# Kernel tuning notes

Hardware: AMD Instinct MI355X
Metric: run time of the kernel (lower is better)

## Reference

```python
import jax, jax.numpy as jnp
import numpy as np
import math

B, S, D, H = 2, 2048, 1024, 16
HD = D // H  # 64 head features


def setup_inputs() -> dict:
    key = jax.random.key(0)
    ks = jax.random.split(key, 6)
    x = jax.random.normal(ks[0], (B, S, D), jnp.float32)
    wq = jax.random.normal(ks[1], (D, D), jnp.float32) * 0.02
    wk = jax.random.normal(ks[2], (D, D), jnp.float32) * 0.02
    wv = jax.random.normal(ks[3], (D, D), jnp.float32) * 0.02
    wo = jax.random.normal(ks[4], (D, D), jnp.float32) * 0.02
    # Llama-style RoPE frequencies: unit-modulus complex per (pos, pair),
    # stored as separate cos/sin arrays of shape [S, HD//2].
    inv_freq = 1.0 / (10000.0 ** (jnp.arange(0, HD, 2, dtype=jnp.float32) / HD))
    ang = jnp.arange(S, dtype=jnp.float32)[:, None] * inv_freq[None, :]
    freq_cos = jnp.cos(ang)
    freq_sin = jnp.sin(ang)
    # realistic padding: each sequence keeps a random prefix of at least S//2 tokens
    lengths = jax.random.randint(ks[5], (B,), S // 2, S + 1)
    padding_mask = (jnp.arange(S)[None, :] < lengths[:, None]).astype(jnp.int32)
    return dict(x=x, wq=wq, wk=wk, wv=wv, wo=wo,
                freq_cos=freq_cos, freq_sin=freq_sin, padding_mask=padding_mask)


def _apply_rope(t, cos, sin):
    # t: [B, S, H, HD]; cos/sin: [S, HD//2]
    tr = t.reshape(t.shape[:-1] + (HD // 2, 2))
    t0, t1 = tr[..., 0], tr[..., 1]
    c = cos[None, :, None, :]
    s = sin[None, :, None, :]
    o0 = t0 * c - t1 * s  # real part of complex multiply
    o1 = t0 * s + t1 * c  # imag part
    return jnp.stack([o0, o1], axis=-1).reshape(t.shape)


def reference(x, wq, wk, wv, wo, freq_cos, freq_sin, padding_mask):
    # QKV projections (torch Linear: y = x @ W.T, no bias)
    q = (x @ wq.T).reshape(B, S, H, HD)
    k = (x @ wk.T).reshape(B, S, H, HD)
    v = (x @ wv.T).reshape(B, S, H, HD)
    q = _apply_rope(q, freq_cos, freq_sin)
    k = _apply_rope(k, freq_cos, freq_sin)
    q = jnp.transpose(q, (0, 2, 1, 3))  # [B,H,S,HD]
    k = jnp.transpose(k, (0, 2, 1, 3))
    v = jnp.transpose(v, (0, 2, 1, 3))
    # NOTE: original scales by sqrt(n_features), not sqrt(head_dim)
    scores = jnp.einsum('bhqd,bhkd->bhqk', q, k) / math.sqrt(D)
    bias = jnp.where(padding_mask[:, None, None, :] == 0,
                     jnp.float32(-jnp.inf), jnp.float32(0.0))
    p = jax.nn.softmax(scores + bias, axis=-1)
    out = jnp.einsum('bhqk,bhkd->bhqd', p, v)
    out = jnp.transpose(out, (0, 2, 1, 3)).reshape(B, S, D)
    return out @ wo.T
```

## Files before the change

kernel.cpp:

```cpp
#include <hip/hip_runtime.h>
#include <hip/hip_bf16.h>
#include <stdint.h>

typedef unsigned short u16;
typedef __attribute__((ext_vector_type(8))) short bf16x8;
typedef __attribute__((ext_vector_type(4))) float f32x4;
typedef __attribute__((ext_vector_type(16))) float f32x16;

__device__ __forceinline__ u16 f2bf(float f) {
  union { float f; uint32_t u; } a; a.f = f;
  return (u16)((a.u + 0x7FFFu + ((a.u >> 16) & 1u)) >> 16);
}

__device__ __forceinline__ void gload_lds16(const void* g, void* l) {
  auto* gp = (__attribute__((address_space(1))) void*)(uintptr_t)g;
  auto* lp = (__attribute__((address_space(3))) void*)(uintptr_t)l;
  __builtin_amdgcn_global_load_lds(gp, lp, 16, 0, 0);
}

__device__ __forceinline__ float exp2_fast(float x) {
  float r;
  asm("v_exp_f32 %0, %1" : "=v"(r) : "v"(x));
  return r;
}

#define CVTPK(d, a, b) asm("v_cvt_pk_bf16_f32 %0, %1, %2" : "=v"(d) : "v"(a), "v"(b))
#define SWAP32(a, b)   asm("v_permlane32_swap_b32 %0, %1" : "+v"(a), "+v"(b))

__global__ void cvt_kernel(const float4* __restrict__ x, const float4* __restrict__ wq,
                           const float4* __restrict__ wk, const float4* __restrict__ wv,
                           const float4* __restrict__ wo,
                           ushort4* __restrict__ xb, ushort4* __restrict__ wqkv,
                           ushort4* __restrict__ wob) {
  const int XN = (2 * 2048 * 1024) / 4;
  const int WN = (1024 * 1024) / 4;
  const int total = XN + 4 * WN;
  for (int i = blockIdx.x * 256 + threadIdx.x; i < total; i += gridDim.x * 256) {
    float4 v; ushort4* dst;
    if (i < XN) { v = x[i]; dst = xb + i; }
    else {
      int j = i - XN; int m = j >> 18; int o = j & (WN - 1);
      const float4* src = (m == 0) ? wq : (m == 1) ? wk : (m == 2) ? wv : wo;
      v = src[o];
      dst = (m < 3) ? (wqkv + j) : (wob + o);
    }
    ushort4 r; r.x = f2bf(v.x); r.y = f2bf(v.y); r.z = f2bf(v.z); r.w = f2bf(v.w);
    *dst = r;
  }
}

__global__ void len_kernel(const int* __restrict__ mask, int* __restrict__ lens) {
  __shared__ int red[256];
  int b = blockIdx.x, s = 0;
  for (int i = threadIdx.x; i < 2048; i += 256) s += mask[b * 2048 + i];
  red[threadIdx.x] = s;
  __syncthreads();
  if (threadIdx.x < 64) {
    int v = red[threadIdx.x] + red[threadIdx.x + 64] + red[threadIdx.x + 128] + red[threadIdx.x + 192];
    #pragma unroll
    for (int o = 32; o > 0; o >>= 1) v += __shfl_down(v, o);
    if (threadIdx.x == 0) lens[b] = v;
  }
}

template <int MODE>
__global__ __launch_bounds__(256, 2)
void gemm_bt(const u16* __restrict__ A, const u16* __restrict__ Bm,
             int M, int N, float* __restrict__ outf,
             u16* __restrict__ Qb, u16* __restrict__ Kb, u16* __restrict__ VbT,
             const float* __restrict__ cosT, const float* __restrict__ sinT) {
  const int K = 1024;
  __shared__ alignas(16) u16 Alds[128 * 32];
  __shared__ alignas(16) u16 Blds[128 * 32];
  const int tid = threadIdx.x, lane = tid & 63, wid = tid >> 6;
  const int nTm = M >> 7;
  const int m0 = (blockIdx.x % nTm) << 7;
  const int n0 = (blockIdx.x / nTm) << 7;
  const int wm = (wid >> 1) << 6, wn = (wid & 1) << 6;
  const int lr = lane & 15, lg = lane >> 4;

  f32x4 acc[4][4];
  #pragma unroll
  for (int i = 0; i < 4; ++i)
    #pragma unroll
    for (int j = 0; j < 4; ++j)
      #pragma unroll
      for (int e = 0; e < 4; ++e) acc[i][j][e] = 0.0f;

  const int r4 = tid >> 2, c4 = (tid & 3) * 8;
  const u16* ag0 = A + (int64_t)(m0 + r4) * K + c4;
  const u16* ag1 = A + (int64_t)(m0 + 64 + r4) * K + c4;
  const u16* bg0 = Bm + (int64_t)(n0 + r4) * K + c4;
  const u16* bg1 = Bm + (int64_t)(n0 + 64 + r4) * K + c4;
  u16* al0 = &Alds[(tid & 192) * 8];
  u16* al1 = &Alds[(256 + (tid & 192)) * 8];
  u16* bl0 = &Blds[(tid & 192) * 8];
  u16* bl1 = &Blds[(256 + (tid & 192)) * 8];

  for (int kt = 0; kt < K / 32; ++kt) {
    const int ko = kt * 32;
    gload_lds16(ag0 + ko, al0);
    gload_lds16(ag1 + ko, al1);
    gload_lds16(bg0 + ko, bl0);
    gload_lds16(bg1 + ko, bl1);
    __syncthreads();
    bf16x8 af[4], bfm[4];
    #pragma unroll
    for (int i = 0; i < 4; ++i) af[i] = *(const bf16x8*)&Alds[(wm + i * 16 + lr) * 32 + lg * 8];
    #pragma unroll
    for (int i = 0; i < 4; ++i) bfm[i] = *(const bf16x8*)&Blds[(wn + i * 16 + lr) * 32 + lg * 8];
    #pragma unroll
    for (int mi = 0; mi < 4; ++mi)
      #pragma unroll
      for (int ni = 0; ni < 4; ++ni)
        acc[mi][ni] = __builtin_amdgcn_mfma_f32_16x16x32_bf16(af[mi], bfm[ni], acc[mi][ni], 0, 0, 0);
    __syncthreads();
  }

  if (MODE == 0) {
    #pragma unroll
    for (int mi = 0; mi < 4; ++mi)
      #pragma unroll
      for (int r = 0; r < 4; ++r) {
        const int row = m0 + wm + mi * 16 + lg * 4 + r;
        float* orow = outf + (int64_t)row * N + n0 + wn + lr;
        #pragma unroll
        for (int ni = 0; ni < 4; ++ni) orow[ni * 16] = acc[mi][ni][r];
      }
  } else {
    #pragma unroll
    for (int mi = 0; mi < 4; ++mi) {
      #pragma unroll
      for (int r = 0; r < 4; ++r) {
        const int row = m0 + wm + mi * 16 + lg * 4 + r;
        const int bb = row >> 11, ss = row & 2047;
        #pragma unroll
        for (int ni = 0; ni < 4; ++ni) {
          const int n = n0 + wn + ni * 16 + lr;
          float v = acc[mi][ni][r];
          if (n < 2048) {
            float partner = __shfl_xor(v, 1);
            const int ii = (n >> 1) & 31;
            const float c = cosT[ss * 32 + ii];
            const float sn = sinT[ss * 32 + ii];
            float rv = (n & 1) ? (partner * sn + v * c) : (v * c - partner * sn);
            const int h = (n >> 6) & 15, d = n & 63;
            const int idx = ((bb * 16 + h) * 2048 + ss) * 64 + d;
            if (n < 1024) Qb[idx] = f2bf(rv * 0.0450842298f);
            else          Kb[idx] = f2bf(rv);
          } else {
            const int n2 = n - 2048;
            const int h = n2 >> 6, d = n2 & 63;
            VbT[((int64_t)(bb * 16 + h) * 64 + d) * 2048 + ss] = f2bf(v);
          }
        }
      }
    }
  }
}

__global__ __launch_bounds__(256, 2)
void attn_kernel(const u16* __restrict__ Qb, const u16* __restrict__ Kb,
                 const u16* __restrict__ VbT, u16* __restrict__ attnb,
                 const int* __restrict__ lens) {
  __shared__ alignas(16) u16 Klds[2][64 * 64];
  __shared__ alignas(16) u16 Vlds[2][64 * 64];
  const int tid = threadIdx.x, lane = tid & 63, wid = tid >> 6;
  const int hi = lane >> 5, ql = lane & 31;
  const int bh = blockIdx.x >> 4;
  const int len = lens[bh >> 4];
  const int qrow = (blockIdx.x & 15) * 128 + wid * 32 + ql;

  bf16x8 qf[4];
  const u16* qptr = Qb + ((int64_t)bh * 2048 + qrow) * 64 + hi * 8;
  #pragma unroll
  for (int c = 0; c < 4; ++c) qf[c] = *(const bf16x8*)(qptr + c * 16);

  const int srow = tid >> 3, schunk = (tid & 7) ^ (srow & 7);
  const u16* kg = Kb + ((int64_t)bh * 2048 + srow) * 64 + schunk * 8;
  const u16* vg = VbT + ((int64_t)bh * 64 + srow) * 2048 + schunk * 8;
  const int dstoff = wid * 512;

  f32x16 oacc[2];
  #pragma unroll
  for (int r = 0; r < 16; ++r) { oacc[0][r] = 0.0f; oacc[1][r] = 0.0f; }
  float mrun = -1e30f, lrun = 0.0f;

  const int nt = (len + 63) >> 6;
  gload_lds16(kg,             &Klds[0][dstoff]);
  gload_lds16(kg + 32 * 64,   &Klds[0][2048 + dstoff]);
  gload_lds16(vg,             &Vlds[0][dstoff]);
  gload_lds16(vg + 32 * 2048, &Vlds[0][2048 + dstoff]);
  __syncthreads();

  const u16* kgn = kg + 64 * 64;
  const u16* vgn = vg + 64;

  for (int t = 0; t < nt; ++t) {
    const int bu = t & 1;
    if (t + 1 < nt) {
      gload_lds16(kgn,             &Klds[bu ^ 1][dstoff]);
      gload_lds16(kgn + 32 * 64,   &Klds[bu ^ 1][2048 + dstoff]);
      gload_lds16(vgn,             &Vlds[bu ^ 1][dstoff]);
      gload_lds16(vgn + 32 * 2048, &Vlds[bu ^ 1][2048 + dstoff]);
    }
    kgn += 64 * 64; vgn += 64;

    f32x16 s0, s1;
    #pragma unroll
    for (int r = 0; r < 16; ++r) { s0[r] = 0.0f; s1[r] = 0.0f; }
    __builtin_amdgcn_s_setprio(1);
    #pragma unroll
    for (int c = 0; c < 4; ++c) {
      const int slot = (((2 * c + hi) ^ (ql & 7)) * 8);
      bf16x8 kf0 = *(const bf16x8*)&Klds[bu][ql * 64 + slot];
      bf16x8 kf1 = *(const bf16x8*)&Klds[bu][(32 + ql) * 64 + slot];
      s0 = __builtin_amdgcn_mfma_f32_32x32x16_bf16(kf0, qf[c], s0, 0, 0, 0);
      s1 = __builtin_amdgcn_mfma_f32_32x32x16_bf16(kf1, qf[c], s1, 0, 0, 0);
    }
    __builtin_amdgcn_s_setprio(0);

    const int k0 = t * 64;
    if (k0 + 64 > len) {
      #pragma unroll
      for (int r = 0; r < 16; ++r) {
        const int key = k0 + (r & 3) + 8 * (r >> 2) + 4 * hi;
        if (key >= len) s0[r] = -1e30f;
        if (key + 32 >= len) s1[r] = -1e30f;
      }
    }

    float ma = fmaxf(s0[0], s1[0]), mb = fmaxf(s0[1], s1[1]);
    float mc = fmaxf(s0[2], s1[2]), md = fmaxf(s0[3], s1[3]);
    #pragma unroll
    for (int r = 4; r < 16; r += 4) {
      ma = fmaxf(ma, fmaxf(s0[r], s1[r]));
      mb = fmaxf(mb, fmaxf(s0[r + 1], s1[r + 1]));
      mc = fmaxf(mc, fmaxf(s0[r + 2], s1[r + 2]));
      md = fmaxf(md, fmaxf(s0[r + 3], s1[r + 3]));
    }
    float mx = fmaxf(fmaxf(ma, mb), fmaxf(mc, md));
    mx = fmaxf(mx, __shfl_xor(mx, 32));
    if (!__all(mx - mrun <= 11.0f)) {
      const float mnew = fmaxf(mrun, mx);
      const float sc = exp2_fast(mrun - mnew);
      #pragma unroll
      for (int r = 0; r < 16; ++r) { oacc[0][r] *= sc; oacc[1][r] *= sc; }
      lrun *= sc;
      mrun = mnew;
    }
    float p[32];
    float ps0 = 0.0f, ps1 = 0.0f, ps2 = 0.0f, ps3 = 0.0f;
    #pragma unroll
    for (int r = 0; r < 16; r += 4) {
      p[r]      = exp2_fast(s0[r] - mrun);
      p[r + 1]  = exp2_fast(s0[r + 1] - mrun);
      p[r + 2]  = exp2_fast(s0[r + 2] - mrun);
      p[r + 3]  = exp2_fast(s0[r + 3] - mrun);
      p[16 + r]     = exp2_fast(s1[r] - mrun);
      p[16 + r + 1] = exp2_fast(s1[r + 1] - mrun);
      p[16 + r + 2] = exp2_fast(s1[r + 2] - mrun);
      p[16 + r + 3] = exp2_fast(s1[r + 3] - mrun);
      ps0 += p[r] + p[16 + r];
      ps1 += p[r + 1] + p[16 + r + 1];
      ps2 += p[r + 2] + p[16 + r + 2];
      ps3 += p[r + 3] + p[16 + r + 3];
    }
    float psum = (ps0 + ps1) + (ps2 + ps3);
    psum += __shfl_xor(psum, 32);
    lrun += psum;

    bf16x8 pfrag[4];
    #pragma unroll
    for (int ks = 0; ks < 4; ++ks) {
      uint32_t a0, a1, a2, a3;
      CVTPK(a0, p[8 * ks + 0], p[8 * ks + 1]);
      CVTPK(a1, p[8 * ks + 2], p[8 * ks + 3]);
      CVTPK(a2, p[8 * ks + 4], p[8 * ks + 5]);
      CVTPK(a3, p[8 * ks + 6], p[8 * ks + 7]);
      SWAP32(a0, a2);
      SWAP32(a1, a3);
      union { uint32_t u[4]; bf16x8 v; } pw;
      pw.u[0] = a0; pw.u[1] = a1; pw.u[2] = a2; pw.u[3] = a3;
      pfrag[ks] = pw.v;
    }

    __builtin_amdgcn_s_setprio(1);
    #pragma unroll
    for (int dc = 0; dc < 2; ++dc) {
      const int drow = dc * 32 + ql;
      #pragma unroll
      for (int ks = 0; ks < 4; ++ks) {
        const int slot = (((2 * ks + hi) ^ (ql & 7)) * 8);
        bf16x8 vf = *(const bf16x8*)&Vlds[bu][drow * 64 + slot];
        oacc[dc] = __builtin_amdgcn_mfma_f32_32x32x16_bf16(vf, pfrag[ks], oacc[dc], 0, 0, 0);
      }
    }
    __builtin_amdgcn_s_setprio(0);
    __syncthreads();
  }

  const float inv = 1.0f / lrun;
  u16* outp = attnb + ((int64_t)((bh >> 4) * 2048 + qrow)) * 1024 + (bh & 15) * 64;
  #pragma unroll
  for (int dc = 0; dc < 2; ++dc)
    #pragma unroll
    for (int g = 0; g < 4; ++g) {
      ushort4 w;
      w.x = f2bf(oacc[dc][4 * g + 0] * inv);
      w.y = f2bf(oacc[dc][4 * g + 1] * inv);
      w.z = f2bf(oacc[dc][4 * g + 2] * inv);
      w.w = f2bf(oacc[dc][4 * g + 3] * inv);
      *(ushort4*)(outp + dc * 32 + 8 * g + 4 * hi) = w;
    }
}

extern "C" void kernel_launch(void* const* d_in, const int* in_sizes, int n_in,
                              void* d_out, int out_size, void* d_ws, size_t ws_size,
                              hipStream_t stream) {
  const float* x    = (const float*)d_in[0];
  const float* wq   = (const float*)d_in[1];
  const float* wk   = (const float*)d_in[2];
  const float* wv   = (const float*)d_in[3];
  const float* wo   = (const float*)d_in[4];
  const float* fcos = (const float*)d_in[5];
  const float* fsin = (const float*)d_in[6];
  const int*   pmsk = (const int*)d_in[7];
  float* out = (float*)d_out;

  char* ws = (char*)d_ws;
  u16* XB    = (u16*)(ws);
  u16* WQKV  = (u16*)(ws + (size_t)8  * 1048576);
  u16* WOB   = (u16*)(ws + (size_t)14 * 1048576);
  u16* QB    = (u16*)(ws + (size_t)16 * 1048576);
  u16* KB    = (u16*)(ws + (size_t)24 * 1048576);
  u16* VBT   = (u16*)(ws + (size_t)32 * 1048576);
  u16* ATTNB = (u16*)(ws + (size_t)40 * 1048576);
  int* LENS  = (int*)(ws + (size_t)48 * 1048576);

  cvt_kernel<<<2048, 256, 0, stream>>>((const float4*)x, (const float4*)wq,
                                       (const float4*)wk, (const float4*)wv,
                                       (const float4*)wo, (ushort4*)XB,
                                       (ushort4*)WQKV, (ushort4*)WOB);
  len_kernel<<<2, 256, 0, stream>>>(pmsk, LENS);
  gemm_bt<1><<<768, 256, 0, stream>>>(XB, WQKV, 4096, 3072, nullptr,
                                      QB, KB, VBT, fcos, fsin);
  attn_kernel<<<512, 256, 0, stream>>>(QB, KB, VBT, ATTNB, LENS);
  gemm_bt<0><<<256, 256, 0, stream>>>(ATTNB, WOB, 4096, 1024, out,
                                      nullptr, nullptr, nullptr, nullptr, nullptr);
}
```

Measured before the change: 122.5 us.

## Replace GEMMs with 8-wave double-buffered swizzled-LDS kernel and split-K output projection

Replaces the simple 128x128 GEMM with an 8-wave, 512-thread kernel. It uses 256-wide N tiles and K=64 steps, XOR-swizzled LDS staging, double buffering with interleaved global-to-LDS loads and MFMA quads, setprio, and XCD-aware block remapping. The QKV projection uses 256x256 tiles. The output projection uses 128x256 tiles with split-K over two slices, accumulated with float atomics after a memset. The aim is to raise MFMA utilisation and hide load latency. In exchange it adds an extra memset, atomic traffic, and non-deterministic summation order.

```diff
diff --git a/kernel.cpp b/kernel.cpp
--- a/kernel.cpp
+++ b/kernel.cpp
@@ -26,6 +26,8 @@
 
 #define CVTPK(d, a, b) asm("v_cvt_pk_bf16_f32 %0, %1, %2" : "=v"(d) : "v"(a), "v"(b))
 #define SWAP32(a, b)   asm("v_permlane32_swap_b32 %0, %1" : "+v"(a), "+v"(b))
+#define BARRIER() do { asm volatile("" ::: "memory"); __builtin_amdgcn_s_barrier(); asm volatile("" ::: "memory"); } while (0)
+#define WAITVM(n) asm volatile("s_waitcnt vmcnt(" #n ")" ::: "memory")
 
 __global__ void cvt_kernel(const float4* __restrict__ x, const float4* __restrict__ wq,
                            const float4* __restrict__ wk, const float4* __restrict__ wv,
@@ -63,80 +65,144 @@
   }
 }
 
-template <int MODE>
-__global__ __launch_bounds__(256, 2)
-void gemm_bt(const u16* __restrict__ A, const u16* __restrict__ Bm,
-             int M, int N, float* __restrict__ outf,
-             u16* __restrict__ Qb, u16* __restrict__ Kb, u16* __restrict__ VbT,
-             const float* __restrict__ cosT, const float* __restrict__ sinT) {
-  const int K = 1024;
-  __shared__ alignas(16) u16 Alds[128 * 32];
-  __shared__ alignas(16) u16 Blds[128 * 32];
+template <int BM, int MODE>
+__global__ __launch_bounds__(512, 2)
+void gemm8(const u16* __restrict__ A, const u16* __restrict__ Bm,
+           int nTm, int nit,
+           float* __restrict__ outf,
+           u16* __restrict__ Qb, u16* __restrict__ Kb, u16* __restrict__ VbT,
+           const float* __restrict__ cosT, const float* __restrict__ sinT) {
+  constexpr int MREP = BM / 32;
+  constexpr int MH   = MREP / 2;
+  constexpr int HA   = BM / 2;
+  constexpr int LA   = BM / 128;
+  extern __shared__ __align__(16) u16 lds[];
+  u16* SA = lds;
+  u16* SB = lds + 2 * BM * 64;
+
   const int tid = threadIdx.x, lane = tid & 63, wid = tid >> 6;
-  const int nTm = M >> 7;
-  const int m0 = (blockIdx.x % nTm) << 7;
-  const int n0 = (blockIdx.x / nTm) << 7;
-  const int wm = (wid >> 1) << 6, wn = (wid & 1) << 6;
+  const int wm = wid >> 2, wn = wid & 3;
   const int lr = lane & 15, lg = lane >> 4;
 
-  f32x4 acc[4][4];
+  const int cpx = gridDim.x >> 3;
+  const int bid = (blockIdx.x & 7) * cpx + (blockIdx.x >> 3);
+  const int m0 = (bid % nTm) * BM;
+  const int n0 = (bid / nTm) * 256;
+  const int kt0 = blockIdx.y * nit * 2;
+
+  const int srow = tid >> 3;
+  const int sslot = (tid & 7) ^ (srow & 7);
+  const u16* gA = A + (int64_t)(m0 + srow) * 1024 + sslot * 8 + kt0 * 64;
+  const u16* gB = Bm + (int64_t)(n0 + srow) * 1024 + sslot * 8 + kt0 * 64;
+  const int sdst = wid * 512;
+
+#define STAGE_A(h, kt) do { \
+    _Pragma("unroll") for (int j = 0; j < LA; ++j) \
+      gload_lds16(gA + (int64_t)((h) * HA + j * 64) * 1024 + (kt) * 64, \
+                  &SA[(((kt) & 1) * BM + (h) * HA) * 64 + sdst + j * 4096]); } while (0)
+#define STAGE_B(h, kt) do { \
+    _Pragma("unroll") for (int j = 0; j < 2; ++j) \
+      gload_lds16(gB + (int64_t)((h) * 128 + j * 64) * 1024 + (kt) * 64, \
+                  &SB[(((kt) & 1) * 256 + (h) * 128) * 64 + sdst + j * 4096]); } while (0)
+#define RD_A(par, mh, dst) do { \
+    _Pragma("unroll") for (int mi = 0; mi < MH; ++mi) \
+    _Pragma("unroll") for (int ks = 0; ks < 2; ++ks) { \
+      const int row = wm * HA + (mh) * (BM / 4) + mi * 16 + lr; \
+      dst[mi][ks] = *(const bf16x8*)&SA[((par) * BM + row) * 64 + (((ks * 4 + lg) ^ (row & 7)) * 8)]; } } while (0)
+#define RD_B(par, nh, dst) do { \
+    _Pragma("unroll") for (int nj = 0; nj < 2; ++nj) \
+    _Pragma("unroll") for (int ks = 0; ks < 2; ++ks) { \
+      const int row = wn * 64 + (nh) * 32 + nj * 16 + lr; \
+      dst[nj][ks] = *(const bf16x8*)&SB[((par) * 256 + row) * 64 + (((ks * 4 + lg) ^ (row & 7)) * 8)]; } } while (0)
+#define QUAD(mh, nh, af, bf) do { \
+    __builtin_amdgcn_s_setprio(1); \
+    _Pragma("unroll") for (int ks = 0; ks < 2; ++ks) \
+    _Pragma("unroll") for (int mi = 0; mi < MH; ++mi) \
+    _Pragma("unroll") for (int nj = 0; nj < 2; ++nj) \
+      acc[(mh) * MH + mi][(nh) * 2 + nj] = __builtin_amdgcn_mfma_f32_16x16x32_bf16( \
+          af[mi][ks], bf[nj][ks], acc[(mh) * MH + mi][(nh) * 2 + nj], 0, 0, 0); \
+    __builtin_amdgcn_s_setprio(0); } while (0)
+
+  f32x4 acc[MREP][4];
   #pragma unroll
-  for (int i = 0; i < 4; ++i)
+  for (int i = 0; i < MREP; ++i)
     #pragma unroll
     for (int j = 0; j < 4; ++j)
       #pragma unroll
       for (int e = 0; e < 4; ++e) acc[i][j][e] = 0.0f;
 
-  const int r4 = tid >> 2, c4 = (tid & 3) * 8;
-  const u16* ag0 = A + (int64_t)(m0 + r4) * K + c4;
-  const u16* ag1 = A + (int64_t)(m0 + 64 + r4) * K + c4;
-  const u16* bg0 = Bm + (int64_t)(n0 + r4) * K + c4;
-  const u16* bg1 = Bm + (int64_t)(n0 + 64 + r4) * K + c4;
-  u16* al0 = &Alds[(tid & 192) * 8];
-  u16* al1 = &Alds[(256 + (tid & 192)) * 8];
-  u16* bl0 = &Blds[(tid & 192) * 8];
-  u16* bl1 = &Blds[(256 + (tid & 192)) * 8];
-
-  for (int kt = 0; kt < K / 32; ++kt) {
-    const int ko = kt * 32;
-    gload_lds16(ag0 + ko, al0);
-    gload_lds16(ag1 + ko, al1);
-    gload_lds16(bg0 + ko, bl0);
-    gload_lds16(bg1 + ko, bl1);
-    __syncthreads();
-    bf16x8 af[4], bfm[4];
-    #pragma unroll
-    for (int i = 0; i < 4; ++i) af[i] = *(const bf16x8*)&Alds[(wm + i * 16 + lr) * 32 + lg * 8];
-    #pragma unroll
-    for (int i = 0; i < 4; ++i) bfm[i] = *(const bf16x8*)&Blds[(wn + i * 16 + lr) * 32 + lg * 8];
-    #pragma unroll
-    for (int mi = 0; mi < 4; ++mi)
-      #pragma unroll
-      for (int ni = 0; ni < 4; ++ni)
-        acc[mi][ni] = __builtin_amdgcn_mfma_f32_16x16x32_bf16(af[mi], bfm[ni], acc[mi][ni], 0, 0, 0);
-    __syncthreads();
+  STAGE_A(0, 0); STAGE_A(1, 0);
+  STAGE_B(0, 0); STAGE_B(1, 0);
+  STAGE_B(0, 1); STAGE_B(1, 1);
+  WAITVM(4);
+  BARRIER();
+
+  for (int u = 0; u < nit; ++u) {
+    const int kt = 2 * u;
+    const bool pf = (u + 1 < nit);
+    bf16x8 a0[MH][2], a1[MH][2], b0[2][2], b1[2][2];
+    RD_A(0, 0, a0); RD_B(0, 0, b0);
+    STAGE_A(0, kt + 1);
+    BARRIER();
+    QUAD(0, 0, a0, b0);
+    BARRIER();
+    RD_B(0, 1, b1);
+    STAGE_A(1, kt + 1);
+    BARRIER();
+    QUAD(0, 1, a0, b1);
+    BARRIER();
+    RD_A(0, 1, a1);
+    if (pf) STAGE_B(0, kt + 2);
+    BARRIER();
+    QUAD(1, 1, a1, b1);
+    BARRIER();
+    if (pf) { STAGE_B(1, kt + 2); WAITVM(4); } else { WAITVM(0); }
+    BARRIER();
+    QUAD(1, 0, a1, b0);
+    BARRIER();
+    RD_A(1, 0, a0); RD_B(1, 0, b0);
+    if (pf) STAGE_A(0, kt + 2);
+    BARRIER();
+    QUAD(0, 0, a0, b0);
+    BARRIER();
+    RD_B(1, 1, b1);
+    if (pf) STAGE_A(1, kt + 2);
+    BARRIER();
+    QUAD(0, 1, a0, b1);
+    BARRIER();
+    RD_A(1, 1, a1);
+    if (pf) STAGE_B(0, kt + 3);
+    BARRIER();
+    QUAD(1, 1, a1, b1);
+    BARRIER();
+    if (pf) { STAGE_B(1, kt + 3); WAITVM(4); } else { WAITVM(0); }
+    BARRIER();
+    QUAD(1, 0, a1, b0);
+    BARRIER();
   }
 
   if (MODE == 0) {
     #pragma unroll
-    for (int mi = 0; mi < 4; ++mi)
+    for (int mi = 0; mi < MREP; ++mi)
       #pragma unroll
       for (int r = 0; r < 4; ++r) {
-        const int row = m0 + wm + mi * 16 + lg * 4 + r;
-        float* orow = outf + (int64_t)row * N + n0 + wn + lr;
+        const int row = m0 + wm * HA + mi * 16 + lg * 4 + r;
         #pragma unroll
-        for (int ni = 0; ni < 4; ++ni) orow[ni * 16] = acc[mi][ni][r];
+        for (int ni = 0; ni < 4; ++ni) {
+          const int col = n0 + wn * 64 + ni * 16 + lr;
+          atomicAdd(outf + (int64_t)row * 1024 + col, acc[mi][ni][r]);
+        }
       }
   } else {
     #pragma unroll
-    for (int mi = 0; mi < 4; ++mi) {
+    for (int mi = 0; mi < MREP; ++mi) {
       #pragma unroll
       for (int r = 0; r < 4; ++r) {
-        const int row = m0 + wm + mi * 16 + lg * 4 + r;
+        const int row = m0 + wm * HA + mi * 16 + lg * 4 + r;
         const int bb = row >> 11, ss = row & 2047;
         #pragma unroll
         for (int ni = 0; ni < 4; ++ni) {
-          const int n = n0 + wn + ni * 16 + lr;
+          const int n = n0 + wn * 64 + ni * 16 + lr;
           float v = acc[mi][ni][r];
           if (n < 2048) {
             float partner = __shfl_xor(v, 1);
@@ -157,6 +223,11 @@
       }
     }
   }
+#undef STAGE_A
+#undef STAGE_B
+#undef RD_A
+#undef RD_B
+#undef QUAD
 }
 
 __global__ __launch_bounds__(256, 2)
@@ -338,14 +409,24 @@
   u16* ATTNB = (u16*)(ws + (size_t)40 * 1048576);
   int* LENS  = (int*)(ws + (size_t)48 * 1048576);
 
+  hipFuncSetAttribute((const void*)gemm8<256, 1>,
+                      hipFuncAttributeMaxDynamicSharedMemorySize, 131072);
+  hipFuncSetAttribute((const void*)gemm8<128, 0>,
+                      hipFuncAttributeMaxDynamicSharedMemorySize, 98304);
+
   cvt_kernel<<<2048, 256, 0, stream>>>((const float4*)x, (const float4*)wq,
                                        (const float4*)wk, (const float4*)wv,
                                        (const float4*)wo, (ushort4*)XB,
                                        (ushort4*)WQKV, (ushort4*)WOB);
   len_kernel<<<2, 256, 0, stream>>>(pmsk, LENS);
-  gemm_bt<1><<<768, 256, 0, stream>>>(XB, WQKV, 4096, 3072, nullptr,
-                                      QB, KB, VBT, fcos, fsin);
+
+  gemm8<256, 1><<<192, 512, 131072, stream>>>(XB, WQKV, 16, 8, nullptr,
+                                              QB, KB, VBT, fcos, fsin);
+
   attn_kernel<<<512, 256, 0, stream>>>(QB, KB, VBT, ATTNB, LENS);
-  gemm_bt<0><<<256, 256, 0, stream>>>(ATTNB, WOB, 4096, 1024, out,
-                                      nullptr, nullptr, nullptr, nullptr, nullptr);
-}
+
+  hipMemsetAsync(out, 0, (size_t)4096 * 1024 * 4, stream);
+  gemm8<128, 0><<<dim3(128, 2), 512, 98304, stream>>>(ATTNB, WOB, 32, 4, out,
+                                                      nullptr, nullptr, nullptr,
+                                                      nullptr, nullptr);
+}
```

Measured after the change: 148.2 us. 1.21x slower.

## Double-buffer GEMM LDS loads with swizzle, XCD-aware block remap, smaller output tiles

Applied to the files above, without the earlier changes.

Replaces the single-buffered GEMM with a templated kernel. It prefetches the next K-slice into a second LDS buffer while MFMAs run on the current one, and XOR-swizzles LDS chunks to cut bank conflicts. It also remaps block IDs so neighbouring tiles land on the same XCD for L2 reuse, raises occupancy hints, and raises MFMA priority. The output projection uses 128x64 tiles so 512 blocks fill the GPU. In exchange it uses more LDS per block and adds manual waitcnt/barrier handling.

```diff
diff --git a/kernel.cpp b/kernel.cpp
--- a/kernel.cpp
+++ b/kernel.cpp
@@ -26,6 +26,8 @@
 
 #define CVTPK(d, a, b) asm("v_cvt_pk_bf16_f32 %0, %1, %2" : "=v"(d) : "v"(a), "v"(b))
 #define SWAP32(a, b)   asm("v_permlane32_swap_b32 %0, %1" : "+v"(a), "+v"(b))
+#define BARRIER() do { asm volatile("" ::: "memory"); __builtin_amdgcn_s_barrier(); asm volatile("" ::: "memory"); } while (0)
+#define WAITVM0() asm volatile("s_waitcnt vmcnt(0)" ::: "memory")
 
 __global__ void cvt_kernel(const float4* __restrict__ x, const float4* __restrict__ wq,
                            const float4* __restrict__ wk, const float4* __restrict__ wv,
@@ -63,79 +65,93 @@
   }
 }
 
-template <int MODE>
-__global__ __launch_bounds__(256, 2)
-void gemm_bt(const u16* __restrict__ A, const u16* __restrict__ Bm,
-             int M, int N, float* __restrict__ outf,
-             u16* __restrict__ Qb, u16* __restrict__ Kb, u16* __restrict__ VbT,
-             const float* __restrict__ cosT, const float* __restrict__ sinT) {
-  const int K = 1024;
-  __shared__ alignas(16) u16 Alds[128 * 32];
-  __shared__ alignas(16) u16 Blds[128 * 32];
+template <int BM, int BN, int MODE>
+__global__ __launch_bounds__(256, 4)
+void gemm2(const u16* __restrict__ A, const u16* __restrict__ Bm,
+           int nTm, float* __restrict__ outf,
+           u16* __restrict__ Qb, u16* __restrict__ Kb, u16* __restrict__ VbT,
+           const float* __restrict__ cosT, const float* __restrict__ sinT) {
+  constexpr int MREP = BM / 32;
+  constexpr int NREP = BN / 32;
+  constexpr int LA = BM / 64;
+  constexpr int LB = BN / 64;
+  __shared__ alignas(16) u16 SA[2][BM * 32];
+  __shared__ alignas(16) u16 SB[2][BN * 32];
+
   const int tid = threadIdx.x, lane = tid & 63, wid = tid >> 6;
-  const int nTm = M >> 7;
-  const int m0 = (blockIdx.x % nTm) << 7;
-  const int n0 = (blockIdx.x / nTm) << 7;
-  const int wm = (wid >> 1) << 6, wn = (wid & 1) << 6;
+  const int wm = (wid >> 1) * (BM / 2), wn = (wid & 1) * (BN / 2);
   const int lr = lane & 15, lg = lane >> 4;
 
-  f32x4 acc[4][4];
+  const int cpx = gridDim.x >> 3;
+  const int bid = (blockIdx.x & 7) * cpx + (blockIdx.x >> 3);
+  const int m0 = (bid % nTm) * BM;
+  const int n0 = (bid / nTm) * BN;
+
+  const int srow = tid >> 2;
+  const int schunk = (tid & 3) ^ (srow & 3);
+  const u16* gA = A + (int64_t)(m0 + srow) * 1024 + schunk * 8;
+  const u16* gB = Bm + (int64_t)(n0 + srow) * 1024 + schunk * 8;
+  const int sdst = wid * 512;
+
+#define STAGE(t) do { const int _b = (t) & 1, _ko = (t) * 32; \
+    _Pragma("unroll") for (int j = 0; j < LA; ++j) \
+      gload_lds16(gA + (int64_t)(j * 64) * 1024 + _ko, &SA[_b][j * 2048 + sdst]); \
+    _Pragma("unroll") for (int j = 0; j < LB; ++j) \
+      gload_lds16(gB + (int64_t)(j * 64) * 1024 + _ko, &SB[_b][j * 2048 + sdst]); } while (0)
+
+  f32x4 acc[MREP][NREP];
   #pragma unroll
-  for (int i = 0; i < 4; ++i)
-    #pragma unroll
-    for (int j = 0; j < 4; ++j)
+  for (int i = 0; i < MREP; ++i)
+    #pragma unroll
+    for (int j = 0; j < NREP; ++j)
       #pragma unroll
       for (int e = 0; e < 4; ++e) acc[i][j][e] = 0.0f;
 
-  const int r4 = tid >> 2, c4 = (tid & 3) * 8;
-  const u16* ag0 = A + (int64_t)(m0 + r4) * K + c4;
-  const u16* ag1 = A + (int64_t)(m0 + 64 + r4) * K + c4;
-  const u16* bg0 = Bm + (int64_t)(n0 + r4) * K + c4;
-  const u16* bg1 = Bm + (int64_t)(n0 + 64 + r4) * K + c4;
-  u16* al0 = &Alds[(tid & 192) * 8];
-  u16* al1 = &Alds[(256 + (tid & 192)) * 8];
-  u16* bl0 = &Blds[(tid & 192) * 8];
-  u16* bl1 = &Blds[(256 + (tid & 192)) * 8];
-
-  for (int kt = 0; kt < K / 32; ++kt) {
-    const int ko = kt * 32;
-    gload_lds16(ag0 + ko, al0);
-    gload_lds16(ag1 + ko, al1);
-    gload_lds16(bg0 + ko, bl0);
-    gload_lds16(bg1 + ko, bl1);
-    __syncthreads();
-    bf16x8 af[4], bfm[4];
-    #pragma unroll
-    for (int i = 0; i < 4; ++i) af[i] = *(const bf16x8*)&Alds[(wm + i * 16 + lr) * 32 + lg * 8];
-    #pragma unroll
-    for (int i = 0; i < 4; ++i) bfm[i] = *(const bf16x8*)&Blds[(wn + i * 16 + lr) * 32 + lg * 8];
-    #pragma unroll
-    for (int mi = 0; mi < 4; ++mi)
-      #pragma unroll
-      for (int ni = 0; ni < 4; ++ni)
+  const int rchunk = (lg ^ (lr & 3)) * 8;
+
+  STAGE(0);
+  WAITVM0();
+  BARRIER();
+
+  for (int t = 0; t < 32; ++t) {
+    if (t < 31) STAGE(t + 1);
+    const u16* sa = SA[t & 1];
+    const u16* sb = SB[t & 1];
+    bf16x8 af[MREP], bfm[NREP];
+    #pragma unroll
+    for (int i = 0; i < MREP; ++i) af[i] = *(const bf16x8*)&sa[(wm + i * 16 + lr) * 32 + rchunk];
+    #pragma unroll
+    for (int i = 0; i < NREP; ++i) bfm[i] = *(const bf16x8*)&sb[(wn + i * 16 + lr) * 32 + rchunk];
+    __builtin_amdgcn_s_setprio(1);
+    #pragma unroll
+    for (int mi = 0; mi < MREP; ++mi)
+      #pragma unroll
+      for (int ni = 0; ni < NREP; ++ni)
         acc[mi][ni] = __builtin_amdgcn_mfma_f32_16x16x32_bf16(af[mi], bfm[ni], acc[mi][ni], 0, 0, 0);
-    __syncthreads();
+    __builtin_amdgcn_s_setprio(0);
+    WAITVM0();
+    BARRIER();
   }
 
   if (MODE == 0) {
     #pragma unroll
-    for (int mi = 0; mi < 4; ++mi)
+    for (int mi = 0; mi < MREP; ++mi)
       #pragma unroll
       for (int r = 0; r < 4; ++r) {
         const int row = m0 + wm + mi * 16 + lg * 4 + r;
-        float* orow = outf + (int64_t)row * N + n0 + wn + lr;
+        float* orow = outf + (int64_t)row * 1024 + n0 + wn + lr;
         #pragma unroll
-        for (int ni = 0; ni < 4; ++ni) orow[ni * 16] = acc[mi][ni][r];
+        for (int ni = 0; ni < NREP; ++ni) orow[ni * 16] = acc[mi][ni][r];
       }
   } else {
     #pragma unroll
-    for (int mi = 0; mi < 4; ++mi) {
+    for (int mi = 0; mi < MREP; ++mi) {
       #pragma unroll
       for (int r = 0; r < 4; ++r) {
         const int row = m0 + wm + mi * 16 + lg * 4 + r;
         const int bb = row >> 11, ss = row & 2047;
         #pragma unroll
-        for (int ni = 0; ni < 4; ++ni) {
+        for (int ni = 0; ni < NREP; ++ni) {
           const int n = n0 + wn + ni * 16 + lr;
           float v = acc[mi][ni][r];
           if (n < 2048) {
@@ -157,6 +173,7 @@
       }
     }
   }
+#undef STAGE
 }
 
 __global__ __launch_bounds__(256, 2)
@@ -343,9 +360,12 @@
                                        (const float4*)wo, (ushort4*)XB,
                                        (ushort4*)WQKV, (ushort4*)WOB);
   len_kernel<<<2, 256, 0, stream>>>(pmsk, LENS);
-  gemm_bt<1><<<768, 256, 0, stream>>>(XB, WQKV, 4096, 3072, nullptr,
-                                      QB, KB, VBT, fcos, fsin);
+
+  gemm2<128, 128, 1><<<768, 256, 0, stream>>>(XB, WQKV, 32, nullptr,
+                                              QB, KB, VBT, fcos, fsin);
+
   attn_kernel<<<512, 256, 0, stream>>>(QB, KB, VBT, ATTNB, LENS);
-  gemm_bt<0><<<256, 256, 0, stream>>>(ATTNB, WOB, 4096, 1024, out,
-                                      nullptr, nullptr, nullptr, nullptr, nullptr);
-}
+
+  gemm2<128, 64, 0><<<512, 256, 0, stream>>>(ATTNB, WOB, 32, out,
+                                             nullptr, nullptr, nullptr, nullptr, nullptr);
+}
```

Result: no change. 124.5 us (+1.7%).
